# Kernel tuning notes

Hardware: AMD Instinct MI355X
Metric: run time of the kernel (lower is better)

The kernel has to match this reference:

```python
import jax, jax.numpy as jnp
import numpy as np

B, S, D = 8, 2048, 1024


def setup_inputs() -> dict:
    key = jax.random.key(0)
    ks = jax.random.split(key, 9)
    s = 1.0 / np.sqrt(D)
    return {
        "x": jax.random.normal(ks[0], (B, S, D), dtype=jnp.float32),
        "Wq": jax.random.normal(ks[1], (D, D), dtype=jnp.float32) * s,
        "bq": jnp.zeros((D,), dtype=jnp.float32),
        "Wk": jax.random.normal(ks[2], (D, D), dtype=jnp.float32) * s,
        "bk": jnp.zeros((D,), dtype=jnp.float32),
        "Wv": jax.random.normal(ks[3], (D, D), dtype=jnp.float32) * s,
        "bv": jnp.zeros((D,), dtype=jnp.float32),
        "Wo": jax.random.normal(ks[4], (D, D), dtype=jnp.float32) * s,
        "bo": jnp.zeros((D,), dtype=jnp.float32),
    }


def reference(x, Wq, bq, Wk, bk, Wv, bv, Wo, bo):
    # Single-head self-attention with full NxN scores (as in the torch module).
    q = jnp.einsum("bsd,de->bse", x, Wq) + bq
    k = jnp.einsum("bsd,de->bse", x, Wk) + bk
    v = jnp.einsum("bsd,de->bse", x, Wv) + bv
    scores = jnp.einsum("bqd,bkd->bqk", q, k) / jnp.sqrt(jnp.float32(D))
    attn = jax.nn.softmax(scores, axis=-1)
    y = jnp.einsum("bqk,bkd->bqd", attn, v)
    return jnp.einsum("bsd,de->bse", y, Wo) + bo
```

## Files before the change

kernel.cpp:

```cpp
#include <hip/hip_runtime.h>
#include <stdint.h>


using u16 = unsigned short;
using u32 = unsigned int;
using short8  = __attribute__((ext_vector_type(8))) short;
using floatx4 = __attribute__((ext_vector_type(4))) float;

#define GPTR(p) ((__attribute__((address_space(1))) u32*)(p))
#define LPTR(p) ((__attribute__((address_space(3))) u32*)(p))
#define MFMA16 __builtin_amdgcn_mfma_f32_16x16x32_bf16

__device__ __forceinline__ void async_cp16(const void* g, void* l) {
  __builtin_amdgcn_global_load_lds(GPTR(g), LPTR(l), 16, 0, 0);
}

__device__ __forceinline__ u16 f2bf(float f) {
  u32 u = __builtin_bit_cast(u32, f);
  u = (u + 0x7fffu + ((u >> 16) & 1u)) >> 16;
  return (u16)u;
}
__device__ __forceinline__ float bf2f(u16 h) {
  u32 u = ((u32)h) << 16;
  return __builtin_bit_cast(float, u);
}

__device__ __forceinline__ void swz(int gx, int gy, int& bx, int& by) {
  int s = blockIdx.x + gx * blockIdx.y;
  int q = s >> 3;
  by = (s & 7) * (gy >> 3) + q / gx;
  bx = q % gx;
}

__device__ __forceinline__ void gemm_core(
    const u16* __restrict__ A, const u16* __restrict__ B,
    int lda, int ldb, int K, u16* lA, u16* lB, floatx4 acc[4][4])
{
  const int tid  = threadIdx.x;
  const int lane = tid & 63;
  const int w    = tid >> 6;
  const int r8   = lane >> 3;
  const int cg   = (lane & 7) ^ r8;
  const int frow = lane & 15;
  const int fq   = lane >> 4;
  const int wrow = (w >> 1) * 64;
  const int wcol = (w & 1) * 64;

  const u16* gaL = A + (size_t)(w * 32 + r8) * lda + cg * 8;
  const u16* gbL = B + (size_t)(w * 32 + r8) * ldb + cg * 8;
  u16* lAw = lA + (w * 32) * 64;
  u16* lBw = lB + (w * 32) * 64;
  const int x0 = ((0 + fq) ^ (frow & 7)) * 8;
  const int x1 = ((4 + fq) ^ (frow & 7)) * 8;

  for (int k0 = 0; k0 < K; k0 += 64) {
    const u16* ga = gaL + k0;
    const u16* gb = gbL + k0;
#pragma unroll
    for (int t = 0; t < 4; ++t) {
      async_cp16(ga + (size_t)(t * 8) * lda, lAw + t * 8 * 64);
      async_cp16(gb + (size_t)(t * 8) * ldb, lBw + t * 8 * 64);
    }
    __syncthreads();

#pragma unroll
    for (int sub = 0; sub < 2; ++sub) {
      const int xs = sub ? x1 : x0;
      short8 af[4], bfr[4];
#pragma unroll
      for (int i = 0; i < 4; ++i)
        af[i] = *(const short8*)(lA + (wrow + i * 16 + frow) * 64 + xs);
#pragma unroll
      for (int j = 0; j < 4; ++j)
        bfr[j] = *(const short8*)(lB + (wcol + j * 16 + frow) * 64 + xs);
#pragma unroll
      for (int i = 0; i < 4; ++i)
#pragma unroll
        for (int j = 0; j < 4; ++j)
          acc[i][j] = MFMA16(af[i], bfr[j], acc[i][j], 0, 0, 0);
    }
    __syncthreads();
  }
}

__device__ __forceinline__ void gemm256(
    const u16* __restrict__ A, const u16* __restrict__ B,
    int lda, int ldb, int K, u16* smem, floatx4 acc[8][4])
{
  const int tid  = threadIdx.x;
  const int lane = tid & 63;
  const int w    = tid >> 6;
  const int frow = lane & 15;
  const int fq   = lane >> 4;
  const int ha   = w >> 2;
  const int hb   = (w & 3) >> 1;
  const int brow = (w & 1) * 64;
  const int x0 = ((0 + fq) ^ (frow & 7)) * 8;
  const int x1 = ((4 + fq) ^ (frow & 7)) * 8;
  const int sr = tid >> 3, sl = tid & 7;
  const int csw = (sl ^ (sr & 7)) << 3;
  const int nt = K >> 6;

  auto stgA = [&](int t, int h, int s) {
    const u16* g = A + (size_t)(h * 128 + sr) * lda + t * 64 + csw;
    u16* l = smem + s * 16384 + h * 8192 + tid * 8;
    async_cp16(g, l);
    async_cp16(g + (size_t)64 * lda, l + 4096);
  };
  auto stgB = [&](int t, int h, int s) {
    const u16* g = B + (size_t)(h * 128 + sr) * ldb + t * 64 + csw;
    u16* l = smem + 32768 + s * 16384 + h * 8192 + tid * 8;
    async_cp16(g, l);
    async_cp16(g + (size_t)64 * ldb, l + 4096);
  };

  stgA(0, 0, 0); stgA(0, 1, 0); stgB(0, 0, 0); stgB(0, 1, 0);
  if (nt > 1) {
    stgB(1, 0, 1); stgA(1, 0, 1);
    asm volatile("s_waitcnt vmcnt(4)" ::: "memory");
  } else {
    asm volatile("s_waitcnt vmcnt(0)" ::: "memory");
  }
  __builtin_amdgcn_s_barrier();

#pragma unroll 2
  for (int t = 0; t < nt; ++t) {
    const int cur = t & 1, oth = cur ^ 1;
    const u16* lA = smem + cur * 16384 + ha * 8192;
    const u16* lB = smem + 32768 + cur * 16384 + hb * 8192;
    short8 af[4][2], b0[2][2], b1[2][2];

#pragma unroll
    for (int i = 0; i < 4; ++i) {
      af[i][0] = *(const short8*)(lA + (i * 16 + frow) * 64 + x0);
      af[i][1] = *(const short8*)(lA + (i * 16 + frow) * 64 + x1);
    }
#pragma unroll
    for (int j = 0; j < 2; ++j) {
      b0[j][0] = *(const short8*)(lB + (brow + j * 16 + frow) * 64 + x0);
      b0[j][1] = *(const short8*)(lB + (brow + j * 16 + frow) * 64 + x1);
    }
    if (t + 1 < nt) stgA(t + 1, 1, oth);
    asm volatile("s_waitcnt lgkmcnt(8)" ::: "memory");
    __builtin_amdgcn_s_barrier();
    asm volatile("s_waitcnt lgkmcnt(0)" ::: "memory");
    __builtin_amdgcn_s_setprio(1);
#pragma unroll
    for (int kk = 0; kk < 2; ++kk)
#pragma unroll
      for (int i = 0; i < 4; ++i)
#pragma unroll
        for (int j = 0; j < 2; ++j)
          acc[i][j] = MFMA16(af[i][kk], b0[j][kk], acc[i][j], 0, 0, 0);
    __builtin_amdgcn_s_setprio(0);
    __builtin_amdgcn_s_barrier();

#pragma unroll
    for (int j = 0; j < 2; ++j) {
      b1[j][0] = *(const short8*)(lB + (brow + 32 + j * 16 + frow) * 64 + x0);
      b1[j][1] = *(const short8*)(lB + (brow + 32 + j * 16 + frow) * 64 + x1);
    }
    if (t + 1 < nt) stgB(t + 1, 1, oth);
    __builtin_amdgcn_s_barrier();
    asm volatile("s_waitcnt lgkmcnt(0)" ::: "memory");
    __builtin_amdgcn_s_setprio(1);
#pragma unroll
    for (int kk = 0; kk < 2; ++kk)
#pragma unroll
      for (int i = 0; i < 4; ++i)
#pragma unroll
        for (int j = 0; j < 2; ++j)
          acc[i][2 + j] = MFMA16(af[i][kk], b1[j][kk], acc[i][2 + j], 0, 0, 0);
    __builtin_amdgcn_s_setprio(0);
    __builtin_amdgcn_s_barrier();

#pragma unroll
    for (int i = 0; i < 4; ++i) {
      af[i][0] = *(const short8*)(lA + (64 + i * 16 + frow) * 64 + x0);
      af[i][1] = *(const short8*)(lA + (64 + i * 16 + frow) * 64 + x1);
    }
    if (t + 2 < nt) stgB(t + 2, 0, cur);
    __builtin_amdgcn_s_barrier();
    asm volatile("s_waitcnt lgkmcnt(0)" ::: "memory");
    __builtin_amdgcn_s_setprio(1);
#pragma unroll
    for (int kk = 0; kk < 2; ++kk)
#pragma unroll
      for (int i = 0; i < 4; ++i)
#pragma unroll
        for (int j = 0; j < 2; ++j)
          acc[4 + i][2 + j] = MFMA16(af[i][kk], b1[j][kk], acc[4 + i][2 + j], 0, 0, 0);
    __builtin_amdgcn_s_setprio(0);
    __builtin_amdgcn_s_barrier();

    if (t + 2 < nt) {
      stgA(t + 2, 0, cur);
      asm volatile("s_waitcnt vmcnt(4)" ::: "memory");
    } else if (t + 1 < nt) {
      asm volatile("s_waitcnt vmcnt(0)" ::: "memory");
    }
    __builtin_amdgcn_s_barrier();
    __builtin_amdgcn_s_setprio(1);
#pragma unroll
    for (int kk = 0; kk < 2; ++kk)
#pragma unroll
      for (int i = 0; i < 4; ++i)
#pragma unroll
        for (int j = 0; j < 2; ++j)
          acc[4 + i][j] = MFMA16(af[i][kk], b0[j][kk], acc[4 + i][j], 0, 0, 0);
    __builtin_amdgcn_s_setprio(0);
    __builtin_amdgcn_s_barrier();
  }
}

__global__ __launch_bounds__(256) void k_cast_x(const float* __restrict__ x, u16* __restrict__ xb) {
  size_t i = ((size_t)blockIdx.x * 256 + threadIdx.x) * 8;
  float4 a = *(const float4*)(x + i);
  float4 b = *(const float4*)(x + i + 4);
  u16 o[8] __attribute__((aligned(16)));
  o[0] = f2bf(a.x); o[1] = f2bf(a.y); o[2] = f2bf(a.z); o[3] = f2bf(a.w);
  o[4] = f2bf(b.x); o[5] = f2bf(b.y); o[6] = f2bf(b.z); o[7] = f2bf(b.w);
  *(uint4*)(xb + i) = *(const uint4*)o;
}

__global__ __launch_bounds__(256) void k_cast_wt(
    const float* __restrict__ Wq, const float* __restrict__ Wk,
    const float* __restrict__ Wo, const float* __restrict__ Wv,
    u16* __restrict__ WT, u16* __restrict__ Wvb)
{
  __shared__ float t[32][33];
  const int z = blockIdx.z;
  const int c = threadIdx.x & 31, r = threadIdx.x >> 5;
  if (z == 3) {
#pragma unroll
    for (int p = 0; p < 4; ++p) {
      const size_t idx = (size_t)(blockIdx.y * 32 + r + 8 * p) * 1024 + blockIdx.x * 32 + c;
      Wvb[idx] = f2bf(Wv[idx]);
    }
    return;
  }
  const float* W = (z == 0) ? Wq : (z == 1) ? Wk : Wo;
  u16* out = WT + (size_t)z * 1024 * 1024;
#pragma unroll
  for (int p = 0; p < 4; ++p)
    t[r + 8 * p][c] = W[(size_t)(blockIdx.y * 32 + r + 8 * p) * 1024 + blockIdx.x * 32 + c];
  __syncthreads();
#pragma unroll
  for (int p = 0; p < 4; ++p)
    out[(size_t)(blockIdx.x * 32 + r + 8 * p) * 1024 + blockIdx.y * 32 + c] = f2bf(t[c][r + 8 * p]);
}

__global__ __launch_bounds__(256) void k_bvo(
    const float* __restrict__ bv, const float* __restrict__ Wo, float* __restrict__ bvo)
{
  const int nb = blockIdx.x & 3, jc = blockIdx.x >> 2;
  const int n = nb * 256 + threadIdx.x;
  float s = 0.f;
#pragma unroll 4
  for (int j = jc * 64; j < jc * 64 + 64; ++j) s += bv[j] * Wo[(size_t)j * 1024 + n];
  atomicAdd(&bvo[n], s);
}

__global__ __launch_bounds__(256, 4) void k_wvo_part(
    const u16* __restrict__ WoT, const u16* __restrict__ Wvb, float* __restrict__ Pf)
{
  __shared__ u16 lA[8192], lB[8192];
  const int bx = blockIdx.x, by = blockIdx.y, z = blockIdx.z;
  const u16* Am = WoT + (size_t)by * 128 * 1024 + z * 256;
  const u16* Bm = Wvb + (size_t)bx * 128 * 1024 + z * 256;
  floatx4 acc[4][4] = {};
  gemm_core(Am, Bm, 1024, 1024, 256, lA, lB, acc);

  float* out = Pf + (size_t)z * 1024 * 1024;
  const int lane = threadIdx.x & 63, w = threadIdx.x >> 6;
  const int wrow = (w >> 1) * 64, wcol = (w & 1) * 64;
#pragma unroll
  for (int j = 0; j < 4; ++j) {
    const int c = bx * 128 + wcol + j * 16 + (lane & 15);
#pragma unroll
    for (int i = 0; i < 4; ++i) {
      const int m0 = by * 128 + wrow + i * 16 + (lane >> 4) * 4;
#pragma unroll
      for (int r = 0; r < 4; ++r)
        out[(size_t)(m0 + r) * 1024 + c] = acc[i][j][r];
    }
  }
}

__global__ __launch_bounds__(256) void k_wvo_red(
    const float* __restrict__ Pf, u16* __restrict__ WvoT)
{
  const size_t e = ((size_t)blockIdx.x * 256 + threadIdx.x) * 8;
  u16 o[8] __attribute__((aligned(16)));
#pragma unroll
  for (int h = 0; h < 2; ++h) {
    float4 s = *(const float4*)(Pf + e + h * 4);
#pragma unroll
    for (int z = 1; z < 4; ++z) {
      float4 p = *(const float4*)(Pf + (size_t)z * 1024 * 1024 + e + h * 4);
      s.x += p.x; s.y += p.y; s.z += p.z; s.w += p.w;
    }
    o[h * 4 + 0] = f2bf(s.x); o[h * 4 + 1] = f2bf(s.y);
    o[h * 4 + 2] = f2bf(s.z); o[h * 4 + 3] = f2bf(s.w);
  }
  *(uint4*)(WvoT + e) = *(const uint4*)o;
}

__global__ __launch_bounds__(512, 2) void k_qkv2(
    const u16* __restrict__ XB, const u16* __restrict__ WT,
    const float* __restrict__ bq, const float* __restrict__ bk, const float* __restrict__ bvo,
    u16* __restrict__ Q, u16* __restrict__ Kb, u16* __restrict__ Vt)
{
  extern __shared__ __align__(16) u16 smem[];
  int bx, by; swz(4, 64, bx, by);
  const int mode = blockIdx.z;
  const u16* Am = XB + (size_t)by * 256 * 1024;
  const int ws_idx = (mode == 2) ? 3 : mode;
  const u16* Bm = WT + (size_t)ws_idx * 1024 * 1024 + (size_t)bx * 256 * 1024;
  const float* bias = (mode == 0) ? bq : (mode == 1) ? bk : bvo;
  floatx4 acc[8][4] = {};
  gemm256(Am, Bm, 1024, 1024, 1024, smem, acc);

  const int tid = threadIdx.x, lane = tid & 63, w = tid >> 6;
  const int frow = lane & 15, fq = lane >> 4;
  const int wrow = (w >> 2) * 128, wcol = (w & 3) * 64;

  if (mode == 2) {
    u16* scr = smem + w * 8192;
#pragma unroll
    for (int j = 0; j < 4; ++j) {
      const int dl = j * 16 + frow;
      const float bb = bias[bx * 256 + wcol + dl];
#pragma unroll
      for (int i = 0; i < 8; ++i) {
        const int sl_ = i * 16 + fq * 4;
        const u32 lo = (u32)f2bf(acc[i][j][0]  + bb) | ((u32)f2bf(acc[i][j][1] + bb) << 16);
        const u32 hi = (u32)f2bf(acc[i][j][2]  + bb) | ((u32)f2bf(acc[i][j][3] + bb) << 16);
        u32* p = (u32*)(scr + dl * 128 + (((sl_ >> 3) ^ (dl & 15)) << 3) + (sl_ & 7));
        p[0] = lo; p[1] = hi;
      }
    }
    const int b = by >> 3, s0 = (by & 7) * 256;
    const int dq = lane >> 4, cc = lane & 15;
#pragma unroll
    for (int it = 0; it < 16; ++it) {
      const int dl = it * 4 + dq;
      uint4 v = *(const uint4*)(scr + dl * 128 + ((cc ^ (dl & 15)) << 3));
      *(uint4*)(Vt + ((size_t)(b * 1024 + bx * 256 + wcol + dl)) * 2048 + s0 + wrow + cc * 8) = v;
    }
    return;
  }

  float bb4[4];
#pragma unroll
  for (int j = 0; j < 4; ++j) bb4[j] = bias[bx * 256 + wcol + j * 16 + frow];
#pragma unroll
  for (int i = 0; i < 8; ++i) {
#pragma unroll
    for (int r = 0; r < 4; ++r) {
      const size_t m = (size_t)(by * 256 + wrow + i * 16 + fq * 4 + r);
#pragma unroll
      for (int j = 0; j < 4; ++j) {
        const int c = bx * 256 + wcol + j * 16 + frow;
        const float v = acc[i][j][r] + bb4[j];
        if (mode == 0) Q[m * 1024 + c] = f2bf(v * 0.03125f);
        else           Kb[m * 1024 + c] = f2bf(v);
      }
    }
  }
}

__global__ __launch_bounds__(512, 2) void k_scores2(
    const u16* __restrict__ Q, const u16* __restrict__ Kb, u16* __restrict__ P,
    float* __restrict__ rowsum)
{
  extern __shared__ __align__(16) u16 smem[];
  const int id = blockIdx.x;
  const int b = id & 7, rest = id >> 3;
  const int bx = rest & 7, by = rest >> 3;
  const u16* Am = Q  + (size_t)b * 2048 * 1024 + (size_t)by * 256 * 1024;
  const u16* Bm = Kb + (size_t)b * 2048 * 1024 + (size_t)bx * 256 * 1024;
  floatx4 acc[8][4] = {};
  gemm256(Am, Bm, 1024, 1024, 1024, smem, acc);

  u16* Pb = P + (size_t)b * 2048 * 2048;
  const int lane = threadIdx.x & 63, w = threadIdx.x >> 6;
  const int frow = lane & 15, fq = lane >> 4;
  const int wrow = (w >> 2) * 128, wcol = (w & 3) * 64;
#pragma unroll
  for (int i = 0; i < 8; ++i) {
#pragma unroll
    for (int r = 0; r < 4; ++r) {
      const int m = by * 256 + wrow + i * 16 + fq * 4 + r;
      float part = 0.f;
#pragma unroll
      for (int j = 0; j < 4; ++j) {
        const int c = bx * 256 + wcol + j * 16 + frow;
        const float e = __expf(acc[i][j][r]);
        const u16 h = f2bf(e);
        Pb[(size_t)m * 2048 + c] = h;
        part += bf2f(h);
      }
      part += __shfl_xor(part, 1, 64);
      part += __shfl_xor(part, 2, 64);
      part += __shfl_xor(part, 4, 64);
      part += __shfl_xor(part, 8, 64);
      if (frow == 0) atomicAdd(&rowsum[b * 2048 + m], part);
    }
  }
}

__global__ __launch_bounds__(512, 2) void k_pv2(
    const u16* __restrict__ P, const u16* __restrict__ Vt,
    const float* __restrict__ bo, const float* __restrict__ rowsum,
    float* __restrict__ out)
{
  extern __shared__ __align__(16) u16 smem[];
  const int id = blockIdx.x;
  const int b = id & 7, rest = id >> 3;
  const int bx = rest & 3, by = rest >> 2;
  const u16* Am = P  + (size_t)b * 2048 * 2048 + (size_t)by * 256 * 2048;
  const u16* Bm = Vt + (size_t)b * 1024 * 2048 + (size_t)bx * 256 * 2048;
  floatx4 acc[8][4] = {};
  gemm256(Am, Bm, 2048, 2048, 2048, smem, acc);

  float* outb = out + (size_t)b * 2048 * 1024;
  const int lane = threadIdx.x & 63, w = threadIdx.x >> 6;
  const int frow = lane & 15, fq = lane >> 4;
  const int wrow = (w >> 2) * 128, wcol = (w & 3) * 64;
  float bb[4];
#pragma unroll
  for (int j = 0; j < 4; ++j) bb[j] = bo[bx * 256 + wcol + j * 16 + frow];
#pragma unroll
  for (int i = 0; i < 8; ++i) {
#pragma unroll
    for (int r = 0; r < 4; ++r) {
      const int m = by * 256 + wrow + i * 16 + fq * 4 + r;
      const float inv = 1.0f / rowsum[b * 2048 + m];
#pragma unroll
      for (int j = 0; j < 4; ++j) {
        const int c = bx * 256 + wcol + j * 16 + frow;
        outb[(size_t)m * 1024 + c] = acc[i][j][r] * inv + bb[j];
      }
    }
  }
}

extern "C" void kernel_launch(void* const* d_in, const int* in_sizes, int n_in,
                              void* d_out, int out_size, void* d_ws, size_t ws_size,
                              hipStream_t stream) {
  const float* x  = (const float*)d_in[0];
  const float* Wq = (const float*)d_in[1];
  const float* bq = (const float*)d_in[2];
  const float* Wk = (const float*)d_in[3];
  const float* bk = (const float*)d_in[4];
  const float* Wv = (const float*)d_in[5];
  const float* bv = (const float*)d_in[6];
  const float* Wo = (const float*)d_in[7];
  const float* bo = (const float*)d_in[8];
  float* out = (float*)d_out;

  char* ws = (char*)d_ws;
  u16* XB  = (u16*)(ws + 0);
  u16* WT  = (u16*)(ws + 33554432);
  u16* Q   = (u16*)(ws + 41943040);
  u16* Kb  = (u16*)(ws + 75497472);
  u16* Vt  = (u16*)(ws + 109051904);
  u16* P   = (u16*)(ws + 142606336);
  u16* Wvb = Kb;
  float* bvo    = (float*)P;
  float* WvoPf  = (float*)(ws + 142606336 + 4194304);
  float* rowsum = (float*)XB;

  if (ws_size < 209715200) return;

  static int attr_set = 0;
  if (!attr_set) {
    hipFuncSetAttribute(reinterpret_cast<const void*>(k_qkv2),
                        hipFuncAttributeMaxDynamicSharedMemorySize, 131072);
    hipFuncSetAttribute(reinterpret_cast<const void*>(k_scores2),
                        hipFuncAttributeMaxDynamicSharedMemorySize, 131072);
    hipFuncSetAttribute(reinterpret_cast<const void*>(k_pv2),
                        hipFuncAttributeMaxDynamicSharedMemorySize, 131072);
    attr_set = 1;
  }

  k_cast_wt  <<<dim3(32, 32, 4), 256, 0, stream>>>(Wq, Wk, Wo, Wv, WT, Wvb);
  k_cast_x   <<<8192, 256, 0, stream>>>(x, XB);
  hipMemsetAsync(bvo, 0, 1024 * sizeof(float), stream);
  k_bvo      <<<64, 256, 0, stream>>>(bv, Wo, bvo);
  k_wvo_part <<<dim3(8, 8, 4), 256, 0, stream>>>(WT + (size_t)2 * 1024 * 1024, Wvb, WvoPf);
  k_wvo_red  <<<512, 256, 0, stream>>>(WvoPf, WT + (size_t)3 * 1024 * 1024);
  k_qkv2     <<<dim3(4, 64, 3), 512, 131072, stream>>>(XB, WT, bq, bk, bvo, Q, Kb, Vt);
  hipMemsetAsync(rowsum, 0, 16384 * sizeof(float), stream);
  k_scores2  <<<512, 512, 131072, stream>>>(Q, Kb, P, rowsum);
  k_pv2      <<<256, 512, 131072, stream>>>(P, Vt, bo, rowsum, out);
}
```

Before: 402.3 us.

## Software-pipeline LDS fragment reads ahead of MFMA blocks in GEMM main loop

Restructures the GEMM inner loop so that the LDS fragment loads for the next MFMA block are issued right after the current block's MFMAs. That includes prefetching the next tile's A and B fragments at the end of the iteration. The goal is to hide LDS read latency behind matrix math and drop the explicit lgkmcnt waits and one barrier per iteration. It relies on the compiler inserting correct waits and on the buffer-reuse ordering staying race-free, and it raises register pressure.

```diff
diff --git a/kernel.cpp b/kernel.cpp
--- a/kernel.cpp
+++ b/kernel.cpp
@@ -113,6 +113,20 @@
     async_cp16(g, l);
     async_cp16(g + (size_t)64 * ldb, l + 4096);
   };
+  auto rdA = [&](short8 d[4][2], const u16* l, int rbase) {
+#pragma unroll
+    for (int i = 0; i < 4; ++i) {
+      d[i][0] = *(const short8*)(l + (rbase + i * 16 + frow) * 64 + x0);
+      d[i][1] = *(const short8*)(l + (rbase + i * 16 + frow) * 64 + x1);
+    }
+  };
+  auto rdB = [&](short8 d[2][2], const u16* l, int rbase) {
+#pragma unroll
+    for (int j = 0; j < 2; ++j) {
+      d[j][0] = *(const short8*)(l + (rbase + j * 16 + frow) * 64 + x0);
+      d[j][1] = *(const short8*)(l + (rbase + j * 16 + frow) * 64 + x1);
+    }
+  };
 
   stgA(0, 0, 0); stgA(0, 1, 0); stgB(0, 0, 0); stgB(0, 1, 0);
   if (nt > 1) {
@@ -122,28 +136,34 @@
     asm volatile("s_waitcnt vmcnt(0)" ::: "memory");
   }
   __builtin_amdgcn_s_barrier();
+  __builtin_amdgcn_sched_barrier(0);
+
+  short8 aX[4][2], b0f[2][2], b1f[2][2];
+  rdA(aX, smem + ha * 8192, 0);
+  rdB(b0f, smem + 32768 + hb * 8192, brow);
 
 #pragma unroll 2
   for (int t = 0; t < nt; ++t) {
     const int cur = t & 1, oth = cur ^ 1;
     const u16* lA = smem + cur * 16384 + ha * 8192;
     const u16* lB = smem + 32768 + cur * 16384 + hb * 8192;
-    short8 af[4][2], b0[2][2], b1[2][2];
-
-#pragma unroll
-    for (int i = 0; i < 4; ++i) {
-      af[i][0] = *(const short8*)(lA + (i * 16 + frow) * 64 + x0);
-      af[i][1] = *(const short8*)(lA + (i * 16 + frow) * 64 + x1);
-    }
-#pragma unroll
-    for (int j = 0; j < 2; ++j) {
-      b0[j][0] = *(const short8*)(lB + (brow + j * 16 + frow) * 64 + x0);
-      b0[j][1] = *(const short8*)(lB + (brow + j * 16 + frow) * 64 + x1);
-    }
+    const u16* nA = smem + oth * 16384 + ha * 8192;
+    const u16* nB = smem + 32768 + oth * 16384 + hb * 8192;
+
     if (t + 1 < nt) stgA(t + 1, 1, oth);
-    asm volatile("s_waitcnt lgkmcnt(8)" ::: "memory");
+    __builtin_amdgcn_s_setprio(1);
+#pragma unroll
+    for (int kk = 0; kk < 2; ++kk)
+#pragma unroll
+      for (int i = 0; i < 4; ++i)
+#pragma unroll
+        for (int j = 0; j < 2; ++j)
+          acc[i][j] = MFMA16(aX[i][kk], b0f[j][kk], acc[i][j], 0, 0, 0);
+    __builtin_amdgcn_s_setprio(0);
+    rdB(b1f, lB, brow + 32);
     __builtin_amdgcn_s_barrier();
-    asm volatile("s_waitcnt lgkmcnt(0)" ::: "memory");
+
+    if (t + 1 < nt) stgB(t + 1, 1, oth);
     __builtin_amdgcn_s_setprio(1);
 #pragma unroll
     for (int kk = 0; kk < 2; ++kk)
@@ -151,18 +171,12 @@
       for (int i = 0; i < 4; ++i)
 #pragma unroll
         for (int j = 0; j < 2; ++j)
-          acc[i][j] = MFMA16(af[i][kk], b0[j][kk], acc[i][j], 0, 0, 0);
+          acc[i][2 + j] = MFMA16(aX[i][kk], b1f[j][kk], acc[i][2 + j], 0, 0, 0);
     __builtin_amdgcn_s_setprio(0);
+    rdA(aX, lA, 64);
     __builtin_amdgcn_s_barrier();
 
-#pragma unroll
-    for (int j = 0; j < 2; ++j) {
-      b1[j][0] = *(const short8*)(lB + (brow + 32 + j * 16 + frow) * 64 + x0);
-      b1[j][1] = *(const short8*)(lB + (brow + 32 + j * 16 + frow) * 64 + x1);
-    }
-    if (t + 1 < nt) stgB(t + 1, 1, oth);
-    __builtin_amdgcn_s_barrier();
-    asm volatile("s_waitcnt lgkmcnt(0)" ::: "memory");
+    if (t + 2 < nt) stgB(t + 2, 0, cur);
     __builtin_amdgcn_s_setprio(1);
 #pragma unroll
     for (int kk = 0; kk < 2; ++kk)
@@ -170,26 +184,7 @@
       for (int i = 0; i < 4; ++i)
 #pragma unroll
         for (int j = 0; j < 2; ++j)
-          acc[i][2 + j] = MFMA16(af[i][kk], b1[j][kk], acc[i][2 + j], 0, 0, 0);
-    __builtin_amdgcn_s_setprio(0);
-    __builtin_amdgcn_s_barrier();
-
-#pragma unroll
-    for (int i = 0; i < 4; ++i) {
-      af[i][0] = *(const short8*)(lA + (64 + i * 16 + frow) * 64 + x0);
-      af[i][1] = *(const short8*)(lA + (64 + i * 16 + frow) * 64 + x1);
-    }
-    if (t + 2 < nt) stgB(t + 2, 0, cur);
-    __builtin_amdgcn_s_barrier();
-    asm volatile("s_waitcnt lgkmcnt(0)" ::: "memory");
-    __builtin_amdgcn_s_setprio(1);
-#pragma unroll
-    for (int kk = 0; kk < 2; ++kk)
-#pragma unroll
-      for (int i = 0; i < 4; ++i)
-#pragma unroll
-        for (int j = 0; j < 2; ++j)
-          acc[4 + i][2 + j] = MFMA16(af[i][kk], b1[j][kk], acc[4 + i][2 + j], 0, 0, 0);
+          acc[4 + i][2 + j] = MFMA16(aX[i][kk], b1f[j][kk], acc[4 + i][2 + j], 0, 0, 0);
     __builtin_amdgcn_s_setprio(0);
     __builtin_amdgcn_s_barrier();
 
@@ -200,6 +195,7 @@
       asm volatile("s_waitcnt vmcnt(0)" ::: "memory");
     }
     __builtin_amdgcn_s_barrier();
+    __builtin_amdgcn_sched_barrier(0);
     __builtin_amdgcn_s_setprio(1);
 #pragma unroll
     for (int kk = 0; kk < 2; ++kk)
@@ -207,9 +203,12 @@
       for (int i = 0; i < 4; ++i)
 #pragma unroll
         for (int j = 0; j < 2; ++j)
-          acc[4 + i][j] = MFMA16(af[i][kk], b0[j][kk], acc[4 + i][j], 0, 0, 0);
+          acc[4 + i][j] = MFMA16(aX[i][kk], b0f[j][kk], acc[4 + i][j], 0, 0, 0);
     __builtin_amdgcn_s_setprio(0);
-    __builtin_amdgcn_s_barrier();
+    if (t + 1 < nt) {
+      rdA(aX, nA, 0);
+      rdB(b0f, nB, brow);
+    }
   }
 }
 
```

New measurement: 515.0 us. +28.0%, slower.

## Merge preprocessing kernels and drop split-K for the Wv·Wo product

Applied to the files above, without the earlier changes.

Folds the x cast, the weight cast/transpose and the bv·Wo bias product into a single launch, which removes several launches and a memset. The Wvo GEMM now runs without split-K, so the fp32 partial buffer and the reduction kernel go away. In exchange the Wvo GEMM uses only 64 blocks with a longer K loop, and the bias product has 4 blocks, each doing a serial 1024-length loop, which may lengthen the preprocessing tail.

```diff
diff --git a/kernel.cpp b/kernel.cpp
--- a/kernel.cpp
+++ b/kernel.cpp
@@ -213,65 +213,67 @@
   }
 }
 
-__global__ __launch_bounds__(256) void k_cast_x(const float* __restrict__ x, u16* __restrict__ xb) {
-  size_t i = ((size_t)blockIdx.x * 256 + threadIdx.x) * 8;
-  float4 a = *(const float4*)(x + i);
-  float4 b = *(const float4*)(x + i + 4);
-  u16 o[8] __attribute__((aligned(16)));
-  o[0] = f2bf(a.x); o[1] = f2bf(a.y); o[2] = f2bf(a.z); o[3] = f2bf(a.w);
-  o[4] = f2bf(b.x); o[5] = f2bf(b.y); o[6] = f2bf(b.z); o[7] = f2bf(b.w);
-  *(uint4*)(xb + i) = *(const uint4*)o;
-}
-
-__global__ __launch_bounds__(256) void k_cast_wt(
+__global__ __launch_bounds__(256) void k_pre(
+    const float* __restrict__ x,
     const float* __restrict__ Wq, const float* __restrict__ Wk,
     const float* __restrict__ Wo, const float* __restrict__ Wv,
-    u16* __restrict__ WT, u16* __restrict__ Wvb)
-{
-  __shared__ float t[32][33];
-  const int z = blockIdx.z;
-  const int c = threadIdx.x & 31, r = threadIdx.x >> 5;
-  if (z == 3) {
-#pragma unroll
-    for (int p = 0; p < 4; ++p) {
-      const size_t idx = (size_t)(blockIdx.y * 32 + r + 8 * p) * 1024 + blockIdx.x * 32 + c;
-      Wvb[idx] = f2bf(Wv[idx]);
-    }
+    const float* __restrict__ bv,
+    u16* __restrict__ xb, u16* __restrict__ WT, u16* __restrict__ Wvb,
+    float* __restrict__ bvo)
+{
+  const int id = blockIdx.x;
+  if (id < 8192) {
+    size_t i = ((size_t)id * 256 + threadIdx.x) * 8;
+    float4 a = *(const float4*)(x + i);
+    float4 b = *(const float4*)(x + i + 4);
+    u16 o[8] __attribute__((aligned(16)));
+    o[0] = f2bf(a.x); o[1] = f2bf(a.y); o[2] = f2bf(a.z); o[3] = f2bf(a.w);
+    o[4] = f2bf(b.x); o[5] = f2bf(b.y); o[6] = f2bf(b.z); o[7] = f2bf(b.w);
+    *(uint4*)(xb + i) = *(const uint4*)o;
     return;
   }
-  const float* W = (z == 0) ? Wq : (z == 1) ? Wk : Wo;
-  u16* out = WT + (size_t)z * 1024 * 1024;
-#pragma unroll
-  for (int p = 0; p < 4; ++p)
-    t[r + 8 * p][c] = W[(size_t)(blockIdx.y * 32 + r + 8 * p) * 1024 + blockIdx.x * 32 + c];
-  __syncthreads();
-#pragma unroll
-  for (int p = 0; p < 4; ++p)
-    out[(size_t)(blockIdx.x * 32 + r + 8 * p) * 1024 + blockIdx.y * 32 + c] = f2bf(t[c][r + 8 * p]);
-}
-
-__global__ __launch_bounds__(256) void k_bvo(
-    const float* __restrict__ bv, const float* __restrict__ Wo, float* __restrict__ bvo)
-{
-  const int nb = blockIdx.x & 3, jc = blockIdx.x >> 2;
-  const int n = nb * 256 + threadIdx.x;
+  if (id < 12288) {
+    __shared__ float t[32][33];
+    const int id2 = id - 8192;
+    const int z = id2 >> 10, rem = id2 & 1023;
+    const int gy = rem >> 5, gx = rem & 31;
+    const int c = threadIdx.x & 31, r = threadIdx.x >> 5;
+    if (z == 3) {
+#pragma unroll
+      for (int p = 0; p < 4; ++p) {
+        const size_t idx = (size_t)(gy * 32 + r + 8 * p) * 1024 + gx * 32 + c;
+        Wvb[idx] = f2bf(Wv[idx]);
+      }
+      return;
+    }
+    const float* W = (z == 0) ? Wq : (z == 1) ? Wk : Wo;
+    u16* out = WT + (size_t)z * 1024 * 1024;
+#pragma unroll
+    for (int p = 0; p < 4; ++p)
+      t[r + 8 * p][c] = W[(size_t)(gy * 32 + r + 8 * p) * 1024 + gx * 32 + c];
+    __syncthreads();
+#pragma unroll
+    for (int p = 0; p < 4; ++p)
+      out[(size_t)(gx * 32 + r + 8 * p) * 1024 + gy * 32 + c] = f2bf(t[c][r + 8 * p]);
+    return;
+  }
+  const int n = (id - 12288) * 256 + threadIdx.x;
   float s = 0.f;
 #pragma unroll 4
-  for (int j = jc * 64; j < jc * 64 + 64; ++j) s += bv[j] * Wo[(size_t)j * 1024 + n];
-  atomicAdd(&bvo[n], s);
-}
-
-__global__ __launch_bounds__(256, 4) void k_wvo_part(
-    const u16* __restrict__ WoT, const u16* __restrict__ Wvb, float* __restrict__ Pf)
+  for (int j = 0; j < 1024; ++j) s += bv[j] * Wo[(size_t)j * 1024 + n];
+  bvo[n] = s;
+}
+
+__global__ __launch_bounds__(256, 4) void k_wvo(
+    const u16* __restrict__ WoT, const u16* __restrict__ Wvb, u16* __restrict__ WvoT)
 {
   __shared__ u16 lA[8192], lB[8192];
-  const int bx = blockIdx.x, by = blockIdx.y, z = blockIdx.z;
-  const u16* Am = WoT + (size_t)by * 128 * 1024 + z * 256;
-  const u16* Bm = Wvb + (size_t)bx * 128 * 1024 + z * 256;
+  const int bx = blockIdx.x, by = blockIdx.y;
+  const u16* Am = WoT + (size_t)by * 128 * 1024;
+  const u16* Bm = Wvb + (size_t)bx * 128 * 1024;
   floatx4 acc[4][4] = {};
-  gemm_core(Am, Bm, 1024, 1024, 256, lA, lB, acc);
-
-  float* out = Pf + (size_t)z * 1024 * 1024;
+  gemm_core(Am, Bm, 1024, 1024, 1024, lA, lB, acc);
+
   const int lane = threadIdx.x & 63, w = threadIdx.x >> 6;
   const int wrow = (w >> 1) * 64, wcol = (w & 1) * 64;
 #pragma unroll
@@ -282,28 +284,9 @@
       const int m0 = by * 128 + wrow + i * 16 + (lane >> 4) * 4;
 #pragma unroll
       for (int r = 0; r < 4; ++r)
-        out[(size_t)(m0 + r) * 1024 + c] = acc[i][j][r];
-    }
-  }
-}
-
-__global__ __launch_bounds__(256) void k_wvo_red(
-    const float* __restrict__ Pf, u16* __restrict__ WvoT)
-{
-  const size_t e = ((size_t)blockIdx.x * 256 + threadIdx.x) * 8;
-  u16 o[8] __attribute__((aligned(16)));
-#pragma unroll
-  for (int h = 0; h < 2; ++h) {
-    float4 s = *(const float4*)(Pf + e + h * 4);
-#pragma unroll
-    for (int z = 1; z < 4; ++z) {
-      float4 p = *(const float4*)(Pf + (size_t)z * 1024 * 1024 + e + h * 4);
-      s.x += p.x; s.y += p.y; s.z += p.z; s.w += p.w;
-    }
-    o[h * 4 + 0] = f2bf(s.x); o[h * 4 + 1] = f2bf(s.y);
-    o[h * 4 + 2] = f2bf(s.z); o[h * 4 + 3] = f2bf(s.w);
-  }
-  *(uint4*)(WvoT + e) = *(const uint4*)o;
+        WvoT[(size_t)(m0 + r) * 1024 + c] = f2bf(acc[i][j][r]);
+    }
+  }
 }
 
 __global__ __launch_bounds__(512, 2) void k_qkv2(
@@ -469,7 +452,6 @@
   u16* P   = (u16*)(ws + 142606336);
   u16* Wvb = Kb;
   float* bvo    = (float*)P;
-  float* WvoPf  = (float*)(ws + 142606336 + 4194304);
   float* rowsum = (float*)XB;
 
   if (ws_size < 209715200) return;
@@ -485,12 +467,9 @@
     attr_set = 1;
   }
 
-  k_cast_wt  <<<dim3(32, 32, 4), 256, 0, stream>>>(Wq, Wk, Wo, Wv, WT, Wvb);
-  k_cast_x   <<<8192, 256, 0, stream>>>(x, XB);
-  hipMemsetAsync(bvo, 0, 1024 * sizeof(float), stream);
-  k_bvo      <<<64, 256, 0, stream>>>(bv, Wo, bvo);
-  k_wvo_part <<<dim3(8, 8, 4), 256, 0, stream>>>(WT + (size_t)2 * 1024 * 1024, Wvb, WvoPf);
-  k_wvo_red  <<<512, 256, 0, stream>>>(WvoPf, WT + (size_t)3 * 1024 * 1024);
+  k_pre      <<<12292, 256, 0, stream>>>(x, Wq, Wk, Wo, Wv, bv, XB, WT, Wvb, bvo);
+  k_wvo      <<<dim3(8, 8), 256, 0, stream>>>(WT + (size_t)2 * 1024 * 1024, Wvb,
+                                              WT + (size_t)3 * 1024 * 1024);
   k_qkv2     <<<dim3(4, 64, 3), 512, 131072, stream>>>(XB, WT, bq, bk, bvo, Q, Kb, Vt);
   hipMemsetAsync(rowsum, 0, 16384 * sizeof(float), stream);
   k_scores2  <<<512, 512, 131072, stream>>>(Q, Kb, P, rowsum);
```

New measurement: 471.6 us. 1.17x slower.
